# Kernel optimization log

Hardware: AMD Instinct MI355X
Metric: run time of the kernel (lower is better)

## Reference

```python
import jax, jax.numpy as jnp
import numpy as np
from jax import lax

VOCAB, EMB, HID, NCLS, BATCH, SEQ = 32000, 512, 512, 8, 64, 512


def setup_inputs() -> dict:
    key = jax.random.key(0)
    ks = jax.random.split(key, 12)
    s = 0.05
    return {
        "x": jax.random.randint(ks[0], (BATCH, SEQ), 0, VOCAB),
        "emb": jax.random.normal(ks[1], (VOCAB, EMB), jnp.float32) * s,
        "W_ih0": jax.random.normal(ks[2], (HID, EMB), jnp.float32) * s,
        "W_hh0": jax.random.normal(ks[3], (HID, HID), jnp.float32) * s,
        "b_ih0": jax.random.normal(ks[4], (HID,), jnp.float32) * s,
        "b_hh0": jax.random.normal(ks[5], (HID,), jnp.float32) * s,
        "W_ih1": jax.random.normal(ks[6], (HID, HID), jnp.float32) * s,
        "W_hh1": jax.random.normal(ks[7], (HID, HID), jnp.float32) * s,
        "b_ih1": jax.random.normal(ks[8], (HID,), jnp.float32) * s,
        "b_hh1": jax.random.normal(ks[9], (HID,), jnp.float32) * s,
        "fc_W": jax.random.normal(ks[10], (NCLS, HID), jnp.float32) * s,
        "fc_b": jax.random.normal(ks[11], (NCLS,), jnp.float32) * s,
    }


def _rnn_layer(inp, W_ih, W_hh, b_ih, b_hh):
    # inp: [B, S, F]; tanh RNN, batch_first. Precompute input projection once.
    pre = jnp.einsum('bsf,hf->bsh', inp, W_ih) + b_ih + b_hh  # [B,S,H]
    B = inp.shape[0]
    H = W_hh.shape[0]
    h0 = jnp.zeros((B, H), inp.dtype)

    def step(h, p_t):  # p_t: [B,H]
        h = jnp.tanh(p_t + h @ W_hh.T)
        return h, h

    hT, ys = lax.scan(step, h0, pre.transpose(1, 0, 2))  # scan over time
    return ys.transpose(1, 0, 2), hT  # outputs [B,S,H], last hidden [B,H]


def reference(x, emb, W_ih0, W_hh0, b_ih0, b_hh0, W_ih1, W_hh1, b_ih1, b_hh1, fc_W, fc_b):
    xe = emb[x]  # [B,S,E] embedding lookup
    out0, _ = _rnn_layer(xe, W_ih0, W_hh0, b_ih0, b_hh0)
    _, h1 = _rnn_layer(out0, W_ih1, W_hh1, b_ih1, b_hh1)  # hidden[-1]
    return h1 @ fc_W.T + fc_b  # [B, n_class]
```

## Files before the change

kernel.cpp:

```cpp
#include <hip/hip_runtime.h>
#include <stdint.h>


#define BB 64
#define SS 512
#define HH 512

typedef short bf16x8 __attribute__((ext_vector_type(8)));
typedef float f32x4 __attribute__((ext_vector_type(4)));
typedef int i32x4 __attribute__((ext_vector_type(4)));
typedef unsigned int u32;
typedef u32 u32x2 __attribute__((ext_vector_type(2)));

__device__ __forceinline__ unsigned short f2bf(float f) {
  uint32_t u = __builtin_bit_cast(uint32_t, f);
  u += 0x7FFFu + ((u >> 16) & 1u);
  return (unsigned short)(u >> 16);
}
__device__ __forceinline__ float bf2f(unsigned short h) {
  uint32_t u = ((uint32_t)h) << 16;
  return __builtin_bit_cast(float, u);
}
__device__ __forceinline__ int pack2(unsigned short a, unsigned short b) {
  return (int)(unsigned int)a | ((int)(unsigned int)b << 16);
}
__device__ __forceinline__ u32 hipack(u32 a, u32 b) {
  return (a >> 16) | (b & 0xFFFF0000u);
}
__device__ __forceinline__ u32 lopack(u32 a, u32 b) {
  return (a & 0xFFF8u) | ((b & 0xFFF8u) << 16);
}
__device__ __forceinline__ bool tag4(i32x4 v, u32 t) {
  u32 m = (((u32)v[0] ^ t) | ((u32)v[1] ^ t) | ((u32)v[2] ^ t) | ((u32)v[3] ^ t)) & 7u;
  return m == 0u;
}
__device__ __forceinline__ float fast_tanh(float v) {
  float a = __builtin_fabsf(v);
  float e = __expf(-2.0f * a);
  float t = (1.0f - e) / (1.0f + e);
  return __builtin_copysignf(t, v);
}

#define UC_LOAD4(dst, ptr) \
  asm volatile("global_load_dwordx4 %0, %1, off sc0 sc1" : "=v"(dst) : "v"(ptr))
#define UC_LOAD1(dst, ptr) \
  asm volatile("global_load_dword %0, %1, off sc0 sc1" : "=v"(dst) : "v"(ptr))
#define UC_STORE2(ptr, v) \
  asm volatile("global_store_dwordx2 %0, %1, off sc0 sc1" ::"v"(ptr), "v"(v) : "memory")

__global__ __launch_bounds__(512, 2) void k_rnn(
    const int* __restrict__ x, const float* __restrict__ emb,
    const float* __restrict__ Wih0, const float* __restrict__ Whh0,
    const float* __restrict__ bih0, const float* __restrict__ bhh0,
    const float* __restrict__ Wih1, const float* __restrict__ Whh1,
    const float* __restrict__ bih1, const float* __restrict__ bhh1,
    u32* __restrict__ hsl) {
  const int tid = threadIdx.x;
  const int bid = blockIdx.x;
  const int layer = bid >> 5;
  const int lb = bid & 31;
  const int bg = lb >> 3;
  const int c = lb & 7;
  const int wid = tid >> 6;
  const int lane = tid & 63;
  const int kq = wid >> 1;
  const int nh = wid & 1;

  __shared__ __align__(16) unsigned short s_in0[16 * 512];
  __shared__ __align__(16) unsigned short s_Hhi[16 * 512];
  __shared__ __align__(16) unsigned short s_Hlo[16 * 512];
  __shared__ __align__(16) float s_part[4 * 16 * 64];

  const float* Wih = layer ? Wih1 : Wih0;
  const float* Whh = layer ? Whh1 : Whh0;
  const float* bi = layer ? bih1 : bih0;
  const float* bh = layer ? bhh1 : bhh0;

  bf16x8 wih[2][4], whhh[2][4], whhl[2][4];
  {
    const int r16 = lane & 15, kg = lane >> 4;
#pragma unroll
    for (int nt = 0; nt < 2; ++nt) {
#pragma unroll
      for (int kt = 0; kt < 4; ++kt) {
        int row = c * 64 + nh * 32 + nt * 16 + r16;
        int k0 = kq * 128 + kt * 32 + kg * 8;
        const float* p = Wih + row * 512 + k0;
        bf16x8 v;
#pragma unroll
        for (int j = 0; j < 8; ++j) v[j] = (short)f2bf(p[j]);
        wih[nt][kt] = v;
        const float* q = Whh + row * 512 + k0;
        bf16x8 vh, vl;
#pragma unroll
        for (int j = 0; j < 8; ++j) {
          float f = q[j];
          unsigned short h = f2bf(f);
          vh[j] = (short)h;
          vl[j] = (short)f2bf(f - bf2f(h));
        }
        whhh[nt][kt] = vh;
        whhl[nt][kt] = vl;
      }
    }
  }
  float biasv0, biasv1;
  {
    int na = (tid & 31) * 2;
    biasv0 = bi[c * 64 + na] + bh[c * 64 + na];
    biasv1 = bi[c * 64 + na + 1] + bh[c * 64 + na + 1];
  }

  const int r_st = tid >> 5;
  const int ch = tid & 31;

  float4 pf0, pf1, pf2, pf3;
  if (layer == 0) {
    int rid = x[(bg * 16 + r_st) * SS + 0];
    const float4* ep = (const float4*)(emb + (size_t)rid * 512 + ch * 16);
    pf0 = ep[0]; pf1 = ep[1]; pf2 = ep[2]; pf3 = ep[3];
  }

  for (int s = 1; s <= SS; ++s) {
    const u32 exp_h = (u32)((s - 1) & 7);
    const u32* ph = hsl +
        (((size_t)layer * 4 + ((s - 1) & 3)) * 64 + bg * 16 + r_st) * 512 + ch * 16;

    if (layer == 0) {
      i32x4 v0, v1;
      v0[0] = pack2(f2bf(pf0.x), f2bf(pf0.y));
      v0[1] = pack2(f2bf(pf0.z), f2bf(pf0.w));
      v0[2] = pack2(f2bf(pf1.x), f2bf(pf1.y));
      v0[3] = pack2(f2bf(pf1.z), f2bf(pf1.w));
      v1[0] = pack2(f2bf(pf2.x), f2bf(pf2.y));
      v1[1] = pack2(f2bf(pf2.z), f2bf(pf2.w));
      v1[2] = pack2(f2bf(pf3.x), f2bf(pf3.y));
      v1[3] = pack2(f2bf(pf3.z), f2bf(pf3.w));
      *(i32x4*)(s_in0 + r_st * 512 + (((2 * ch) ^ (r_st & 7)) << 3)) = v0;
      *(i32x4*)(s_in0 + r_st * 512 + (((2 * ch + 1) ^ (r_st & 7)) << 3)) = v1;
      if (s < SS) {
        int rid = x[(bg * 16 + r_st) * SS + s];
        const float4* ep = (const float4*)(emb + (size_t)rid * 512 + ch * 16);
        pf0 = ep[0]; pf1 = ep[1]; pf2 = ep[2]; pf3 = ep[3];
      }
    } else {
      i32x4 i0 = {0, 0, 0, 0}, i1 = {0, 0, 0, 0}, i2 = {0, 0, 0, 0}, i3 = {0, 0, 0, 0};
      const u32 exp_i = (u32)(s & 7);
      const u32* pi =
          hsl + (((size_t)(s & 3)) * 64 + bg * 16 + r_st) * 512 + ch * 16;
      while (true) {
        UC_LOAD4(i0, pi);
        UC_LOAD4(i1, pi + 4);
        UC_LOAD4(i2, pi + 8);
        UC_LOAD4(i3, pi + 12);
        asm volatile("s_waitcnt vmcnt(0)"
                     : "+v"(i0), "+v"(i1), "+v"(i2), "+v"(i3)::"memory");
        bool ok = tag4(i0, exp_i) && tag4(i1, exp_i) && tag4(i2, exp_i) &&
                  tag4(i3, exp_i);
        if (__all(ok)) break;
      }
      i32x4 A0 = {(int)hipack(i0[0], i0[1]), (int)hipack(i0[2], i0[3]),
                  (int)hipack(i1[0], i1[1]), (int)hipack(i1[2], i1[3])};
      i32x4 A1 = {(int)hipack(i2[0], i2[1]), (int)hipack(i2[2], i2[3]),
                  (int)hipack(i3[0], i3[1]), (int)hipack(i3[2], i3[3])};
      *(i32x4*)(s_in0 + r_st * 512 + (((2 * ch) ^ (r_st & 7)) << 3)) = A0;
      *(i32x4*)(s_in0 + r_st * 512 + (((2 * ch + 1) ^ (r_st & 7)) << 3)) = A1;
    }
    __syncthreads();

    f32x4 acc0 = {0.f, 0.f, 0.f, 0.f};
    f32x4 acc1 = {0.f, 0.f, 0.f, 0.f};
    {
      const int r16 = lane & 15, kg = lane >> 4;
#pragma unroll
      for (int kt = 0; kt < 4; ++kt) {
        int k8 = kq * 16 + kt * 4 + kg;
        bf16x8 ain = __builtin_bit_cast(
            bf16x8, *(const i32x4*)(s_in0 + r16 * 512 + ((k8 ^ (r16 & 7)) << 3)));
        acc0 = __builtin_amdgcn_mfma_f32_16x16x32_bf16(ain, wih[0][kt], acc0, 0, 0, 0);
        acc1 = __builtin_amdgcn_mfma_f32_16x16x32_bf16(ain, wih[1][kt], acc1, 0, 0, 0);
      }
    }

    if (s > 1) {
      i32x4 h0 = {0, 0, 0, 0}, h1 = {0, 0, 0, 0}, h2 = {0, 0, 0, 0}, h3 = {0, 0, 0, 0};
      if (layer == 0) {
        const bool need_bp = (s > 4) && (tid < 8);
        const u32 exp_bp = (u32)((s - 4) & 7);
        const u32* pbp = hsl + ((size_t)(4 + ((s - 4) & 3)) * 64 + bg * 16) * 512 +
                         (tid < 8 ? tid * 64 : 0);
        while (true) {
          u32 bpw = 0;
          UC_LOAD4(h0, ph);
          UC_LOAD4(h1, ph + 4);
          UC_LOAD4(h2, ph + 8);
          UC_LOAD4(h3, ph + 12);
          UC_LOAD1(bpw, pbp);
          asm volatile("s_waitcnt vmcnt(0)"
                       : "+v"(h0), "+v"(h1), "+v"(h2), "+v"(h3), "+v"(bpw)::"memory");
          bool ok = tag4(h0, exp_h) && tag4(h1, exp_h) && tag4(h2, exp_h) &&
                    tag4(h3, exp_h) && (!need_bp || ((bpw & 7u) == exp_bp));
          if (__all(ok)) break;
        }
      } else {
        while (true) {
          UC_LOAD4(h0, ph);
          UC_LOAD4(h1, ph + 4);
          UC_LOAD4(h2, ph + 8);
          UC_LOAD4(h3, ph + 12);
          asm volatile("s_waitcnt vmcnt(0)"
                       : "+v"(h0), "+v"(h1), "+v"(h2), "+v"(h3)::"memory");
          bool ok = tag4(h0, exp_h) && tag4(h1, exp_h) && tag4(h2, exp_h) &&
                    tag4(h3, exp_h);
          if (__all(ok)) break;
        }
      }
      i32x4 A0 = {(int)hipack(h0[0], h0[1]), (int)hipack(h0[2], h0[3]),
                  (int)hipack(h1[0], h1[1]), (int)hipack(h1[2], h1[3])};
      i32x4 A1 = {(int)hipack(h2[0], h2[1]), (int)hipack(h2[2], h2[3]),
                  (int)hipack(h3[0], h3[1]), (int)hipack(h3[2], h3[3])};
      i32x4 B0 = {(int)lopack(h0[0], h0[1]), (int)lopack(h0[2], h0[3]),
                  (int)lopack(h1[0], h1[1]), (int)lopack(h1[2], h1[3])};
      i32x4 B1v = {(int)lopack(h2[0], h2[1]), (int)lopack(h2[2], h2[3]),
                   (int)lopack(h3[0], h3[1]), (int)lopack(h3[2], h3[3])};
      *(i32x4*)(s_Hhi + r_st * 512 + (((2 * ch) ^ (r_st & 7)) << 3)) = A0;
      *(i32x4*)(s_Hhi + r_st * 512 + (((2 * ch + 1) ^ (r_st & 7)) << 3)) = A1;
      *(i32x4*)(s_Hlo + r_st * 512 + (((2 * ch) ^ (r_st & 7)) << 3)) = B0;
      *(i32x4*)(s_Hlo + r_st * 512 + (((2 * ch + 1) ^ (r_st & 7)) << 3)) = B1v;
    }
    __syncthreads();

    {
      const int r16 = lane & 15, kg = lane >> 4;
      if (s > 1) {
#pragma unroll
        for (int kt = 0; kt < 4; ++kt) {
          int k8 = kq * 16 + kt * 4 + kg;
          bf16x8 ahi = __builtin_bit_cast(
              bf16x8, *(const i32x4*)(s_Hhi + r16 * 512 + ((k8 ^ (r16 & 7)) << 3)));
          bf16x8 alo = __builtin_bit_cast(
              bf16x8, *(const i32x4*)(s_Hlo + r16 * 512 + ((k8 ^ (r16 & 7)) << 3)));
          acc0 = __builtin_amdgcn_mfma_f32_16x16x32_bf16(ahi, whhh[0][kt], acc0, 0, 0, 0);
          acc0 = __builtin_amdgcn_mfma_f32_16x16x32_bf16(ahi, whhl[0][kt], acc0, 0, 0, 0);
          acc0 = __builtin_amdgcn_mfma_f32_16x16x32_bf16(alo, whhh[0][kt], acc0, 0, 0, 0);
          acc1 = __builtin_amdgcn_mfma_f32_16x16x32_bf16(ahi, whhh[1][kt], acc1, 0, 0, 0);
          acc1 = __builtin_amdgcn_mfma_f32_16x16x32_bf16(ahi, whhl[1][kt], acc1, 0, 0, 0);
          acc1 = __builtin_amdgcn_mfma_f32_16x16x32_bf16(alo, whhh[1][kt], acc1, 0, 0, 0);
        }
      }
#pragma unroll
      for (int j = 0; j < 4; ++j) {
        int m = kg * 4 + j;
        int xr = (m >> 2) & 3;
        int n0i = nh * 32 + 0 * 16 + r16;
        int n1i = nh * 32 + 1 * 16 + r16;
        s_part[kq * 1024 + m * 64 + (n0i ^ (xr << 4))] = acc0[j];
        s_part[kq * 1024 + m * 64 + (n1i ^ (xr << 4))] = acc1[j];
      }
    }
    __syncthreads();

    {
      int m = tid >> 5, na = (tid & 31) * 2;
      int xr = (m >> 2) & 3;
      float v0 = biasv0, v1 = biasv1;
#pragma unroll
      for (int q2 = 0; q2 < 4; ++q2) {
        const float2* sp =
            (const float2*)(s_part + q2 * 1024 + m * 64 + (na ^ (xr << 4)));
        float2 t = *sp;
        v0 += t.x;
        v1 += t.y;
      }
      v0 = fast_tanh(v0);
      v1 = fast_tanh(v1);
      unsigned short a0 = f2bf(v0), a1 = f2bf(v1);
      unsigned short b0 = f2bf(v0 - bf2f(a0)), b1 = f2bf(v1 - bf2f(a1));
      u32 tag = (u32)(s & 7);
      u32x2 wv;
      wv[0] = ((u32)a0 << 16) | ((u32)b0 & 0xFFF8u) | tag;
      wv[1] = ((u32)a1 << 16) | ((u32)b1 & 0xFFF8u) | tag;
      u32* dst = hsl + (((size_t)layer * 4 + (s & 3)) * 64 + bg * 16 + m) * 512 +
                 c * 64 + na;
      UC_STORE2(dst, wv);
    }
  }
}

__global__ void k_fc(const u32* __restrict__ h1w, const float* __restrict__ fcW,
                     const float* __restrict__ fcb, float* __restrict__ out) {
  int i = threadIdx.x;
  int b = i >> 3, cc = i & 7;
  float acc = fcb[cc];
  const u32* ph = h1w + b * 512;
  const float* pw = fcW + cc * 512;
  for (int k = 0; k < 512; k += 4) {
    int4 w4 = *(const int4*)(ph + k);
    float4 wv = *(const float4*)(pw + k);
    acc += (bf2f((unsigned short)((u32)w4.x >> 16)) +
            bf2f((unsigned short)((u32)w4.x & 0xFFF8u))) * wv.x;
    acc += (bf2f((unsigned short)((u32)w4.y >> 16)) +
            bf2f((unsigned short)((u32)w4.y & 0xFFF8u))) * wv.y;
    acc += (bf2f((unsigned short)((u32)w4.z >> 16)) +
            bf2f((unsigned short)((u32)w4.z & 0xFFF8u))) * wv.z;
    acc += (bf2f((unsigned short)((u32)w4.w >> 16)) +
            bf2f((unsigned short)((u32)w4.w & 0xFFF8u))) * wv.w;
  }
  out[b * 8 + cc] = acc;
}

extern "C" void kernel_launch(void* const* d_in, const int* in_sizes, int n_in,
                              void* d_out, int out_size, void* d_ws, size_t ws_size,
                              hipStream_t stream) {
  const int* x = (const int*)d_in[0];
  const float* emb = (const float*)d_in[1];
  const float* Wih0 = (const float*)d_in[2];
  const float* Whh0 = (const float*)d_in[3];
  const float* bih0 = (const float*)d_in[4];
  const float* bhh0 = (const float*)d_in[5];
  const float* Wih1 = (const float*)d_in[6];
  const float* Whh1 = (const float*)d_in[7];
  const float* bih1 = (const float*)d_in[8];
  const float* bhh1 = (const float*)d_in[9];
  const float* fcW = (const float*)d_in[10];
  const float* fcb = (const float*)d_in[11];

  u32* hsl = (u32*)d_ws;

  hipMemsetAsync(hsl, 0, (size_t)2 * 4 * 64 * 512 * 4, stream);
  hipLaunchKernelGGL(k_rnn, dim3(64), dim3(512), 0, stream, x, emb, Wih0, Whh0,
                     bih0, bhh0, Wih1, Whh1, bih1, bhh1, hsl);
  hipLaunchKernelGGL(k_fc, dim3(1), dim3(512), 0, stream,
                     hsl + (size_t)4 * 64 * 512, fcW, fcb, (float*)d_out);
}
```

Measured before the change: 2.071 ms.

## Give each wave full K range to drop cross-wave reduction and barrier

Each block now runs 4 waves instead of 8, and each wave owns 16 output columns across the full 512-wide K dimension, holding 16 k-tiles of each weight matrix in registers. This removes the shared-memory partial-sum buffer, one __syncthreads per timestep and the cross-wave reduction. Each wave writes tanh outputs straight to global memory with per-element dword stores. In exchange, per-thread register use triples, each thread loads twice as much h state per step, and each wave runs a longer serial chain of MFMAs, which may lengthen the per-step critical path.

```diff
diff --git a/kernel.cpp b/kernel.cpp
--- a/kernel.cpp
+++ b/kernel.cpp
@@ -10,7 +10,6 @@
 typedef float f32x4 __attribute__((ext_vector_type(4)));
 typedef int i32x4 __attribute__((ext_vector_type(4)));
 typedef unsigned int u32;
-typedef u32 u32x2 __attribute__((ext_vector_type(2)));
 
 __device__ __forceinline__ unsigned short f2bf(float f) {
   uint32_t u = __builtin_bit_cast(uint32_t, f);
@@ -45,10 +44,10 @@
   asm volatile("global_load_dwordx4 %0, %1, off sc0 sc1" : "=v"(dst) : "v"(ptr))
 #define UC_LOAD1(dst, ptr) \
   asm volatile("global_load_dword %0, %1, off sc0 sc1" : "=v"(dst) : "v"(ptr))
-#define UC_STORE2(ptr, v) \
-  asm volatile("global_store_dwordx2 %0, %1, off sc0 sc1" ::"v"(ptr), "v"(v) : "memory")
-
-__global__ __launch_bounds__(512, 2) void k_rnn(
+#define UC_STORE1(ptr, v) \
+  asm volatile("global_store_dword %0, %1, off sc0 sc1" ::"v"(ptr), "v"(v) : "memory")
+
+__global__ __launch_bounds__(256, 1) void k_rnn(
     const int* __restrict__ x, const float* __restrict__ emb,
     const float* __restrict__ Wih0, const float* __restrict__ Whh0,
     const float* __restrict__ bih0, const float* __restrict__ bhh0,
@@ -63,127 +62,138 @@
   const int c = lb & 7;
   const int wid = tid >> 6;
   const int lane = tid & 63;
-  const int kq = wid >> 1;
-  const int nh = wid & 1;
+  const int r16 = lane & 15, kg = lane >> 4;
 
   __shared__ __align__(16) unsigned short s_in0[16 * 512];
   __shared__ __align__(16) unsigned short s_Hhi[16 * 512];
   __shared__ __align__(16) unsigned short s_Hlo[16 * 512];
-  __shared__ __align__(16) float s_part[4 * 16 * 64];
 
   const float* Wih = layer ? Wih1 : Wih0;
   const float* Whh = layer ? Whh1 : Whh0;
   const float* bi = layer ? bih1 : bih0;
   const float* bh = layer ? bhh1 : bhh0;
 
-  bf16x8 wih[2][4], whhh[2][4], whhl[2][4];
+  bf16x8 wih[16], whhh[16], whhl[16];
   {
-    const int r16 = lane & 15, kg = lane >> 4;
-#pragma unroll
-    for (int nt = 0; nt < 2; ++nt) {
-#pragma unroll
-      for (int kt = 0; kt < 4; ++kt) {
-        int row = c * 64 + nh * 32 + nt * 16 + r16;
-        int k0 = kq * 128 + kt * 32 + kg * 8;
-        const float* p = Wih + row * 512 + k0;
-        bf16x8 v;
-#pragma unroll
-        for (int j = 0; j < 8; ++j) v[j] = (short)f2bf(p[j]);
-        wih[nt][kt] = v;
-        const float* q = Whh + row * 512 + k0;
-        bf16x8 vh, vl;
-#pragma unroll
-        for (int j = 0; j < 8; ++j) {
-          float f = q[j];
-          unsigned short h = f2bf(f);
-          vh[j] = (short)h;
-          vl[j] = (short)f2bf(f - bf2f(h));
-        }
-        whhh[nt][kt] = vh;
-        whhl[nt][kt] = vl;
-      }
-    }
-  }
-  float biasv0, biasv1;
+    const int row = c * 64 + wid * 16 + r16;
+#pragma unroll
+    for (int kt = 0; kt < 16; ++kt) {
+      const int k0 = kt * 32 + kg * 8;
+      const float* p = Wih + row * 512 + k0;
+      bf16x8 v;
+#pragma unroll
+      for (int j = 0; j < 8; ++j) v[j] = (short)f2bf(p[j]);
+      wih[kt] = v;
+      const float* q = Whh + row * 512 + k0;
+      bf16x8 vh, vl;
+#pragma unroll
+      for (int j = 0; j < 8; ++j) {
+        float f = q[j];
+        unsigned short h = f2bf(f);
+        vh[j] = (short)h;
+        vl[j] = (short)f2bf(f - bf2f(h));
+      }
+      whhh[kt] = vh;
+      whhl[kt] = vl;
+    }
+  }
+  float bv;
   {
-    int na = (tid & 31) * 2;
-    biasv0 = bi[c * 64 + na] + bh[c * 64 + na];
-    biasv1 = bi[c * 64 + na + 1] + bh[c * 64 + na + 1];
-  }
-
-  const int r_st = tid >> 5;
-  const int ch = tid & 31;
-
-  float4 pf0, pf1, pf2, pf3;
+    const int gcol = c * 64 + wid * 16 + r16;
+    bv = bi[gcol] + bh[gcol];
+  }
+
+  const int r_st = tid >> 4;
+  const int ch = tid & 15;
+
+  float4 pf0, pf1, pf2, pf3, pf4, pf5, pf6, pf7;
   if (layer == 0) {
     int rid = x[(bg * 16 + r_st) * SS + 0];
-    const float4* ep = (const float4*)(emb + (size_t)rid * 512 + ch * 16);
+    const float4* ep = (const float4*)(emb + (size_t)rid * 512 + ch * 32);
     pf0 = ep[0]; pf1 = ep[1]; pf2 = ep[2]; pf3 = ep[3];
+    pf4 = ep[4]; pf5 = ep[5]; pf6 = ep[6]; pf7 = ep[7];
   }
 
   for (int s = 1; s <= SS; ++s) {
     const u32 exp_h = (u32)((s - 1) & 7);
     const u32* ph = hsl +
-        (((size_t)layer * 4 + ((s - 1) & 3)) * 64 + bg * 16 + r_st) * 512 + ch * 16;
+        (((size_t)layer * 4 + ((s - 1) & 3)) * 64 + bg * 16 + r_st) * 512 + ch * 32;
 
     if (layer == 0) {
-      i32x4 v0, v1;
-      v0[0] = pack2(f2bf(pf0.x), f2bf(pf0.y));
-      v0[1] = pack2(f2bf(pf0.z), f2bf(pf0.w));
-      v0[2] = pack2(f2bf(pf1.x), f2bf(pf1.y));
-      v0[3] = pack2(f2bf(pf1.z), f2bf(pf1.w));
-      v1[0] = pack2(f2bf(pf2.x), f2bf(pf2.y));
-      v1[1] = pack2(f2bf(pf2.z), f2bf(pf2.w));
-      v1[2] = pack2(f2bf(pf3.x), f2bf(pf3.y));
-      v1[3] = pack2(f2bf(pf3.z), f2bf(pf3.w));
-      *(i32x4*)(s_in0 + r_st * 512 + (((2 * ch) ^ (r_st & 7)) << 3)) = v0;
-      *(i32x4*)(s_in0 + r_st * 512 + (((2 * ch + 1) ^ (r_st & 7)) << 3)) = v1;
+      i32x4 v0 = {pack2(f2bf(pf0.x), f2bf(pf0.y)), pack2(f2bf(pf0.z), f2bf(pf0.w)),
+                  pack2(f2bf(pf1.x), f2bf(pf1.y)), pack2(f2bf(pf1.z), f2bf(pf1.w))};
+      i32x4 v1 = {pack2(f2bf(pf2.x), f2bf(pf2.y)), pack2(f2bf(pf2.z), f2bf(pf2.w)),
+                  pack2(f2bf(pf3.x), f2bf(pf3.y)), pack2(f2bf(pf3.z), f2bf(pf3.w))};
+      i32x4 v2 = {pack2(f2bf(pf4.x), f2bf(pf4.y)), pack2(f2bf(pf4.z), f2bf(pf4.w)),
+                  pack2(f2bf(pf5.x), f2bf(pf5.y)), pack2(f2bf(pf5.z), f2bf(pf5.w))};
+      i32x4 v3 = {pack2(f2bf(pf6.x), f2bf(pf6.y)), pack2(f2bf(pf6.z), f2bf(pf6.w)),
+                  pack2(f2bf(pf7.x), f2bf(pf7.y)), pack2(f2bf(pf7.z), f2bf(pf7.w))};
+      *(i32x4*)(s_in0 + r_st * 512 + (((ch * 4 + 0) ^ (r_st & 7)) << 3)) = v0;
+      *(i32x4*)(s_in0 + r_st * 512 + (((ch * 4 + 1) ^ (r_st & 7)) << 3)) = v1;
+      *(i32x4*)(s_in0 + r_st * 512 + (((ch * 4 + 2) ^ (r_st & 7)) << 3)) = v2;
+      *(i32x4*)(s_in0 + r_st * 512 + (((ch * 4 + 3) ^ (r_st & 7)) << 3)) = v3;
       if (s < SS) {
         int rid = x[(bg * 16 + r_st) * SS + s];
-        const float4* ep = (const float4*)(emb + (size_t)rid * 512 + ch * 16);
+        const float4* ep = (const float4*)(emb + (size_t)rid * 512 + ch * 32);
         pf0 = ep[0]; pf1 = ep[1]; pf2 = ep[2]; pf3 = ep[3];
+        pf4 = ep[4]; pf5 = ep[5]; pf6 = ep[6]; pf7 = ep[7];
       }
     } else {
       i32x4 i0 = {0, 0, 0, 0}, i1 = {0, 0, 0, 0}, i2 = {0, 0, 0, 0}, i3 = {0, 0, 0, 0};
+      i32x4 i4 = {0, 0, 0, 0}, i5 = {0, 0, 0, 0}, i6 = {0, 0, 0, 0}, i7 = {0, 0, 0, 0};
       const u32 exp_i = (u32)(s & 7);
       const u32* pi =
-          hsl + (((size_t)(s & 3)) * 64 + bg * 16 + r_st) * 512 + ch * 16;
+          hsl + (((size_t)(s & 3)) * 64 + bg * 16 + r_st) * 512 + ch * 32;
       while (true) {
         UC_LOAD4(i0, pi);
         UC_LOAD4(i1, pi + 4);
         UC_LOAD4(i2, pi + 8);
         UC_LOAD4(i3, pi + 12);
+        UC_LOAD4(i4, pi + 16);
+        UC_LOAD4(i5, pi + 20);
+        UC_LOAD4(i6, pi + 24);
+        UC_LOAD4(i7, pi + 28);
         asm volatile("s_waitcnt vmcnt(0)"
-                     : "+v"(i0), "+v"(i1), "+v"(i2), "+v"(i3)::"memory");
+                     : "+v"(i0), "+v"(i1), "+v"(i2), "+v"(i3), "+v"(i4), "+v"(i5),
+                       "+v"(i6), "+v"(i7)::"memory");
         bool ok = tag4(i0, exp_i) && tag4(i1, exp_i) && tag4(i2, exp_i) &&
-                  tag4(i3, exp_i);
+                  tag4(i3, exp_i) && tag4(i4, exp_i) && tag4(i5, exp_i) &&
+                  tag4(i6, exp_i) && tag4(i7, exp_i);
         if (__all(ok)) break;
       }
       i32x4 A0 = {(int)hipack(i0[0], i0[1]), (int)hipack(i0[2], i0[3]),
                   (int)hipack(i1[0], i1[1]), (int)hipack(i1[2], i1[3])};
       i32x4 A1 = {(int)hipack(i2[0], i2[1]), (int)hipack(i2[2], i2[3]),
                   (int)hipack(i3[0], i3[1]), (int)hipack(i3[2], i3[3])};
-      *(i32x4*)(s_in0 + r_st * 512 + (((2 * ch) ^ (r_st & 7)) << 3)) = A0;
-      *(i32x4*)(s_in0 + r_st * 512 + (((2 * ch + 1) ^ (r_st & 7)) << 3)) = A1;
+      i32x4 A2 = {(int)hipack(i4[0], i4[1]), (int)hipack(i4[2], i4[3]),
+                  (int)hipack(i5[0], i5[1]), (int)hipack(i5[2], i5[3])};
+      i32x4 A3 = {(int)hipack(i6[0], i6[1]), (int)hipack(i6[2], i6[3]),
+                  (int)hipack(i7[0], i7[1]), (int)hipack(i7[2], i7[3])};
+      *(i32x4*)(s_in0 + r_st * 512 + (((ch * 4 + 0) ^ (r_st & 7)) << 3)) = A0;
+      *(i32x4*)(s_in0 + r_st * 512 + (((ch * 4 + 1) ^ (r_st & 7)) << 3)) = A1;
+      *(i32x4*)(s_in0 + r_st * 512 + (((ch * 4 + 2) ^ (r_st & 7)) << 3)) = A2;
+      *(i32x4*)(s_in0 + r_st * 512 + (((ch * 4 + 3) ^ (r_st & 7)) << 3)) = A3;
     }
     __syncthreads();
 
     f32x4 acc0 = {0.f, 0.f, 0.f, 0.f};
     f32x4 acc1 = {0.f, 0.f, 0.f, 0.f};
-    {
-      const int r16 = lane & 15, kg = lane >> 4;
-#pragma unroll
-      for (int kt = 0; kt < 4; ++kt) {
-        int k8 = kq * 16 + kt * 4 + kg;
-        bf16x8 ain = __builtin_bit_cast(
-            bf16x8, *(const i32x4*)(s_in0 + r16 * 512 + ((k8 ^ (r16 & 7)) << 3)));
-        acc0 = __builtin_amdgcn_mfma_f32_16x16x32_bf16(ain, wih[0][kt], acc0, 0, 0, 0);
-        acc1 = __builtin_amdgcn_mfma_f32_16x16x32_bf16(ain, wih[1][kt], acc1, 0, 0, 0);
-      }
+    f32x4 acc2 = {0.f, 0.f, 0.f, 0.f};
+    f32x4 acc3 = {0.f, 0.f, 0.f, 0.f};
+#pragma unroll
+    for (int kt = 0; kt < 16; ++kt) {
+      const int k8 = kt * 4 + kg;
+      bf16x8 ain = __builtin_bit_cast(
+          bf16x8, *(const i32x4*)(s_in0 + r16 * 512 + ((k8 ^ (r16 & 7)) << 3)));
+      if ((kt & 3) == 0) acc0 = __builtin_amdgcn_mfma_f32_16x16x32_bf16(ain, wih[kt], acc0, 0, 0, 0);
+      if ((kt & 3) == 1) acc1 = __builtin_amdgcn_mfma_f32_16x16x32_bf16(ain, wih[kt], acc1, 0, 0, 0);
+      if ((kt & 3) == 2) acc2 = __builtin_amdgcn_mfma_f32_16x16x32_bf16(ain, wih[kt], acc2, 0, 0, 0);
+      if ((kt & 3) == 3) acc3 = __builtin_amdgcn_mfma_f32_16x16x32_bf16(ain, wih[kt], acc3, 0, 0, 0);
     }
 
     if (s > 1) {
       i32x4 h0 = {0, 0, 0, 0}, h1 = {0, 0, 0, 0}, h2 = {0, 0, 0, 0}, h3 = {0, 0, 0, 0};
+      i32x4 h4 = {0, 0, 0, 0}, h5 = {0, 0, 0, 0}, h6 = {0, 0, 0, 0}, h7 = {0, 0, 0, 0};
       if (layer == 0) {
         const bool need_bp = (s > 4) && (tid < 8);
         const u32 exp_bp = (u32)((s - 4) & 7);
@@ -195,11 +205,18 @@
           UC_LOAD4(h1, ph + 4);
           UC_LOAD4(h2, ph + 8);
           UC_LOAD4(h3, ph + 12);
+          UC_LOAD4(h4, ph + 16);
+          UC_LOAD4(h5, ph + 20);
+          UC_LOAD4(h6, ph + 24);
+          UC_LOAD4(h7, ph + 28);
           UC_LOAD1(bpw, pbp);
           asm volatile("s_waitcnt vmcnt(0)"
-                       : "+v"(h0), "+v"(h1), "+v"(h2), "+v"(h3), "+v"(bpw)::"memory");
+                       : "+v"(h0), "+v"(h1), "+v"(h2), "+v"(h3), "+v"(h4), "+v"(h5),
+                         "+v"(h6), "+v"(h7), "+v"(bpw)::"memory");
           bool ok = tag4(h0, exp_h) && tag4(h1, exp_h) && tag4(h2, exp_h) &&
-                    tag4(h3, exp_h) && (!need_bp || ((bpw & 7u) == exp_bp));
+                    tag4(h3, exp_h) && tag4(h4, exp_h) && tag4(h5, exp_h) &&
+                    tag4(h6, exp_h) && tag4(h7, exp_h) &&
+                    (!need_bp || ((bpw & 7u) == exp_bp));
           if (__all(ok)) break;
         }
       } else {
@@ -208,10 +225,16 @@
           UC_LOAD4(h1, ph + 4);
           UC_LOAD4(h2, ph + 8);
           UC_LOAD4(h3, ph + 12);
+          UC_LOAD4(h4, ph + 16);
+          UC_LOAD4(h5, ph + 20);
+          UC_LOAD4(h6, ph + 24);
+          UC_LOAD4(h7, ph + 28);
           asm volatile("s_waitcnt vmcnt(0)"
-                       : "+v"(h0), "+v"(h1), "+v"(h2), "+v"(h3)::"memory");
+                       : "+v"(h0), "+v"(h1), "+v"(h2), "+v"(h3), "+v"(h4), "+v"(h5),
+                         "+v"(h6), "+v"(h7)::"memory");
           bool ok = tag4(h0, exp_h) && tag4(h1, exp_h) && tag4(h2, exp_h) &&
-                    tag4(h3, exp_h);
+                    tag4(h3, exp_h) && tag4(h4, exp_h) && tag4(h5, exp_h) &&
+                    tag4(h6, exp_h) && tag4(h7, exp_h);
           if (__all(ok)) break;
         }
       }
@@ -219,70 +242,73 @@
                   (int)hipack(h1[0], h1[1]), (int)hipack(h1[2], h1[3])};
       i32x4 A1 = {(int)hipack(h2[0], h2[1]), (int)hipack(h2[2], h2[3]),
                   (int)hipack(h3[0], h3[1]), (int)hipack(h3[2], h3[3])};
+      i32x4 A2 = {(int)hipack(h4[0], h4[1]), (int)hipack(h4[2], h4[3]),
+                  (int)hipack(h5[0], h5[1]), (int)hipack(h5[2], h5[3])};
+      i32x4 A3 = {(int)hipack(h6[0], h6[1]), (int)hipack(h6[2], h6[3]),
+                  (int)hipack(h7[0], h7[1]), (int)hipack(h7[2], h7[3])};
       i32x4 B0 = {(int)lopack(h0[0], h0[1]), (int)lopack(h0[2], h0[3]),
                   (int)lopack(h1[0], h1[1]), (int)lopack(h1[2], h1[3])};
       i32x4 B1v = {(int)lopack(h2[0], h2[1]), (int)lopack(h2[2], h2[3]),
                    (int)lopack(h3[0], h3[1]), (int)lopack(h3[2], h3[3])};
-      *(i32x4*)(s_Hhi + r_st * 512 + (((2 * ch) ^ (r_st & 7)) << 3)) = A0;
-      *(i32x4*)(s_Hhi + r_st * 512 + (((2 * ch + 1) ^ (r_st & 7)) << 3)) = A1;
-      *(i32x4*)(s_Hlo + r_st * 512 + (((2 * ch) ^ (r_st & 7)) << 3)) = B0;
-      *(i32x4*)(s_Hlo + r_st * 512 + (((2 * ch + 1) ^ (r_st & 7)) << 3)) = B1v;
+      i32x4 B2v = {(int)lopack(h4[0], h4[1]), (int)lopack(h4[2], h4[3]),
+                   (int)lopack(h5[0], h5[1]), (int)lopack(h5[2], h5[3])};
+      i32x4 B3v = {(int)lopack(h6[0], h6[1]), (int)lopack(h6[2], h6[3]),
+                   (int)lopack(h7[0], h7[1]), (int)lopack(h7[2], h7[3])};
+      *(i32x4*)(s_Hhi + r_st * 512 + (((ch * 4 + 0) ^ (r_st & 7)) << 3)) = A0;
+      *(i32x4*)(s_Hhi + r_st * 512 + (((ch * 4 + 1) ^ (r_st & 7)) << 3)) = A1;
+      *(i32x4*)(s_Hhi + r_st * 512 + (((ch * 4 + 2) ^ (r_st & 7)) << 3)) = A2;
+      *(i32x4*)(s_Hhi + r_st * 512 + (((ch * 4 + 3) ^ (r_st & 7)) << 3)) = A3;
+      *(i32x4*)(s_Hlo + r_st * 512 + (((ch * 4 + 0) ^ (r_st & 7)) << 3)) = B0;
+      *(i32x4*)(s_Hlo + r_st * 512 + (((ch * 4 + 1) ^ (r_st & 7)) << 3)) = B1v;
+      *(i32x4*)(s_Hlo + r_st * 512 + (((ch * 4 + 2) ^ (r_st & 7)) << 3)) = B2v;
+      *(i32x4*)(s_Hlo + r_st * 512 + (((ch * 4 + 3) ^ (r_st & 7)) << 3)) = B3v;
     }
     __syncthreads();
 
+    if (s > 1) {
+#pragma unroll
+      for (int kt = 0; kt < 16; ++kt) {
+        const int k8 = kt * 4 + kg;
+        bf16x8 ahi = __builtin_bit_cast(
+            bf16x8, *(const i32x4*)(s_Hhi + r16 * 512 + ((k8 ^ (r16 & 7)) << 3)));
+        bf16x8 alo = __builtin_bit_cast(
+            bf16x8, *(const i32x4*)(s_Hlo + r16 * 512 + ((k8 ^ (r16 & 7)) << 3)));
+        if ((kt & 3) == 0) {
+          acc0 = __builtin_amdgcn_mfma_f32_16x16x32_bf16(ahi, whhh[kt], acc0, 0, 0, 0);
+          acc0 = __builtin_amdgcn_mfma_f32_16x16x32_bf16(ahi, whhl[kt], acc0, 0, 0, 0);
+          acc0 = __builtin_amdgcn_mfma_f32_16x16x32_bf16(alo, whhh[kt], acc0, 0, 0, 0);
+        }
+        if ((kt & 3) == 1) {
+          acc1 = __builtin_amdgcn_mfma_f32_16x16x32_bf16(ahi, whhh[kt], acc1, 0, 0, 0);
+          acc1 = __builtin_amdgcn_mfma_f32_16x16x32_bf16(ahi, whhl[kt], acc1, 0, 0, 0);
+          acc1 = __builtin_amdgcn_mfma_f32_16x16x32_bf16(alo, whhh[kt], acc1, 0, 0, 0);
+        }
+        if ((kt & 3) == 2) {
+          acc2 = __builtin_amdgcn_mfma_f32_16x16x32_bf16(ahi, whhh[kt], acc2, 0, 0, 0);
+          acc2 = __builtin_amdgcn_mfma_f32_16x16x32_bf16(ahi, whhl[kt], acc2, 0, 0, 0);
+          acc2 = __builtin_amdgcn_mfma_f32_16x16x32_bf16(alo, whhh[kt], acc2, 0, 0, 0);
+        }
+        if ((kt & 3) == 3) {
+          acc3 = __builtin_amdgcn_mfma_f32_16x16x32_bf16(ahi, whhh[kt], acc3, 0, 0, 0);
+          acc3 = __builtin_amdgcn_mfma_f32_16x16x32_bf16(ahi, whhl[kt], acc3, 0, 0, 0);
+          acc3 = __builtin_amdgcn_mfma_f32_16x16x32_bf16(alo, whhh[kt], acc3, 0, 0, 0);
+        }
+      }
+    }
+
     {
-      const int r16 = lane & 15, kg = lane >> 4;
-      if (s > 1) {
-#pragma unroll
-        for (int kt = 0; kt < 4; ++kt) {
-          int k8 = kq * 16 + kt * 4 + kg;
-          bf16x8 ahi = __builtin_bit_cast(
-              bf16x8, *(const i32x4*)(s_Hhi + r16 * 512 + ((k8 ^ (r16 & 7)) << 3)));
-          bf16x8 alo = __builtin_bit_cast(
-              bf16x8, *(const i32x4*)(s_Hlo + r16 * 512 + ((k8 ^ (r16 & 7)) << 3)));
-          acc0 = __builtin_amdgcn_mfma_f32_16x16x32_bf16(ahi, whhh[0][kt], acc0, 0, 0, 0);
-          acc0 = __builtin_amdgcn_mfma_f32_16x16x32_bf16(ahi, whhl[0][kt], acc0, 0, 0, 0);
-          acc0 = __builtin_amdgcn_mfma_f32_16x16x32_bf16(alo, whhh[0][kt], acc0, 0, 0, 0);
-          acc1 = __builtin_amdgcn_mfma_f32_16x16x32_bf16(ahi, whhh[1][kt], acc1, 0, 0, 0);
-          acc1 = __builtin_amdgcn_mfma_f32_16x16x32_bf16(ahi, whhl[1][kt], acc1, 0, 0, 0);
-          acc1 = __builtin_amdgcn_mfma_f32_16x16x32_bf16(alo, whhh[1][kt], acc1, 0, 0, 0);
-        }
-      }
+      f32x4 fa = acc0 + acc1 + acc2 + acc3;
+      const u32 tag = (u32)(s & 7);
+      u32* dst = hsl + (((size_t)layer * 4 + (s & 3)) * 64 + bg * 16 + kg * 4) * 512 +
+                 c * 64 + wid * 16 + r16;
 #pragma unroll
       for (int j = 0; j < 4; ++j) {
-        int m = kg * 4 + j;
-        int xr = (m >> 2) & 3;
-        int n0i = nh * 32 + 0 * 16 + r16;
-        int n1i = nh * 32 + 1 * 16 + r16;
-        s_part[kq * 1024 + m * 64 + (n0i ^ (xr << 4))] = acc0[j];
-        s_part[kq * 1024 + m * 64 + (n1i ^ (xr << 4))] = acc1[j];
-      }
-    }
-    __syncthreads();
-
-    {
-      int m = tid >> 5, na = (tid & 31) * 2;
-      int xr = (m >> 2) & 3;
-      float v0 = biasv0, v1 = biasv1;
-#pragma unroll
-      for (int q2 = 0; q2 < 4; ++q2) {
-        const float2* sp =
-            (const float2*)(s_part + q2 * 1024 + m * 64 + (na ^ (xr << 4)));
-        float2 t = *sp;
-        v0 += t.x;
-        v1 += t.y;
-      }
-      v0 = fast_tanh(v0);
-      v1 = fast_tanh(v1);
-      unsigned short a0 = f2bf(v0), a1 = f2bf(v1);
-      unsigned short b0 = f2bf(v0 - bf2f(a0)), b1 = f2bf(v1 - bf2f(a1));
-      u32 tag = (u32)(s & 7);
-      u32x2 wv;
-      wv[0] = ((u32)a0 << 16) | ((u32)b0 & 0xFFF8u) | tag;
-      wv[1] = ((u32)a1 << 16) | ((u32)b1 & 0xFFF8u) | tag;
-      u32* dst = hsl + (((size_t)layer * 4 + (s & 3)) * 64 + bg * 16 + m) * 512 +
-                 c * 64 + na;
-      UC_STORE2(dst, wv);
+        float t = fast_tanh(fa[j] + bv);
+        unsigned short a = f2bf(t);
+        unsigned short b = f2bf(t - bf2f(a));
+        u32 wv = ((u32)a << 16) | ((u32)b & 0xFFF8u) | tag;
+        UC_STORE1(dst + j * 512, wv);
+      }
     }
   }
 }
@@ -328,7 +354,7 @@
   u32* hsl = (u32*)d_ws;
 
   hipMemsetAsync(hsl, 0, (size_t)2 * 4 * 64 * 512 * 4, stream);
-  hipLaunchKernelGGL(k_rnn, dim3(64), dim3(512), 0, stream, x, emb, Wih0, Whh0,
+  hipLaunchKernelGGL(k_rnn, dim3(64), dim3(256), 0, stream, x, emb, Wih0, Whh0,
                      bih0, bhh0, Wih1, Whh1, bih1, bhh1, hsl);
   hipLaunchKernelGGL(k_fc, dim3(1), dim3(512), 0, stream,
                      hsl + (size_t)4 * 64 * 512, fcW, fcb, (float*)d_out);
```

New measurement: 2.798 ms. 35.1% more time.

## Use LDS-only barriers, split MFMA accumulators, and defer embedding prefetch

Applied to the files above, without the earlier changes.

Three of the per-step __syncthreads calls become an LDS-only wait plus s_barrier, so the barriers no longer wait on outstanding global loads. This lets the embedding prefetch, now issued after the input-projection MFMAs, stay in flight across the barriers. The recurrent MFMAs accumulate into six independent accumulators instead of two serial chains, which shortens dependency latency; the partial sums are added at the end. The risk is different floating-point summation order and more register pressure, though the launch bounds of 512 threads and 2 blocks already constrain registers.

```diff
diff --git a/kernel.cpp b/kernel.cpp
--- a/kernel.cpp
+++ b/kernel.cpp
@@ -40,6 +40,12 @@
   float t = (1.0f - e) / (1.0f + e);
   return __builtin_copysignf(t, v);
 }
+
+#define BAR_LDS()                                            \
+  do {                                                       \
+    asm volatile("s_waitcnt lgkmcnt(0)" ::: "memory");       \
+    __builtin_amdgcn_s_barrier();                            \
+  } while (0)
 
 #define UC_LOAD4(dst, ptr) \
   asm volatile("global_load_dwordx4 %0, %1, off sc0 sc1" : "=v"(dst) : "v"(ptr))
@@ -65,6 +71,7 @@
   const int lane = tid & 63;
   const int kq = wid >> 1;
   const int nh = wid & 1;
+  const int r16 = lane & 15, kg = lane >> 4;
 
   __shared__ __align__(16) unsigned short s_in0[16 * 512];
   __shared__ __align__(16) unsigned short s_Hhi[16 * 512];
@@ -78,7 +85,6 @@
 
   bf16x8 wih[2][4], whhh[2][4], whhl[2][4];
   {
-    const int r16 = lane & 15, kg = lane >> 4;
 #pragma unroll
     for (int nt = 0; nt < 2; ++nt) {
 #pragma unroll
@@ -125,6 +131,9 @@
     const u32 exp_h = (u32)((s - 1) & 7);
     const u32* ph = hsl +
         (((size_t)layer * 4 + ((s - 1) & 3)) * 64 + bg * 16 + r_st) * 512 + ch * 16;
+
+    int nrid = 0;
+    if (layer == 0 && s < SS) nrid = x[(bg * 16 + r_st) * SS + s];
 
     if (layer == 0) {
       i32x4 v0, v1;
@@ -138,11 +147,6 @@
       v1[3] = pack2(f2bf(pf3.z), f2bf(pf3.w));
       *(i32x4*)(s_in0 + r_st * 512 + (((2 * ch) ^ (r_st & 7)) << 3)) = v0;
       *(i32x4*)(s_in0 + r_st * 512 + (((2 * ch + 1) ^ (r_st & 7)) << 3)) = v1;
-      if (s < SS) {
-        int rid = x[(bg * 16 + r_st) * SS + s];
-        const float4* ep = (const float4*)(emb + (size_t)rid * 512 + ch * 16);
-        pf0 = ep[0]; pf1 = ep[1]; pf2 = ep[2]; pf3 = ep[3];
-      }
     } else {
       i32x4 i0 = {0, 0, 0, 0}, i1 = {0, 0, 0, 0}, i2 = {0, 0, 0, 0}, i3 = {0, 0, 0, 0};
       const u32 exp_i = (u32)(s & 7);
@@ -166,22 +170,28 @@
       *(i32x4*)(s_in0 + r_st * 512 + (((2 * ch) ^ (r_st & 7)) << 3)) = A0;
       *(i32x4*)(s_in0 + r_st * 512 + (((2 * ch + 1) ^ (r_st & 7)) << 3)) = A1;
     }
-    __syncthreads();
-
-    f32x4 acc0 = {0.f, 0.f, 0.f, 0.f};
-    f32x4 acc1 = {0.f, 0.f, 0.f, 0.f};
-    {
-      const int r16 = lane & 15, kg = lane >> 4;
-#pragma unroll
-      for (int kt = 0; kt < 4; ++kt) {
-        int k8 = kq * 16 + kt * 4 + kg;
-        bf16x8 ain = __builtin_bit_cast(
-            bf16x8, *(const i32x4*)(s_in0 + r16 * 512 + ((k8 ^ (r16 & 7)) << 3)));
-        acc0 = __builtin_amdgcn_mfma_f32_16x16x32_bf16(ain, wih[0][kt], acc0, 0, 0, 0);
-        acc1 = __builtin_amdgcn_mfma_f32_16x16x32_bf16(ain, wih[1][kt], acc1, 0, 0, 0);
-      }
-    }
-
+    BAR_LDS();
+
+    f32x4 a0i = {0.f, 0.f, 0.f, 0.f};
+    f32x4 a1i = {0.f, 0.f, 0.f, 0.f};
+#pragma unroll
+    for (int kt = 0; kt < 4; ++kt) {
+      int k8 = kq * 16 + kt * 4 + kg;
+      bf16x8 ain = __builtin_bit_cast(
+          bf16x8, *(const i32x4*)(s_in0 + r16 * 512 + ((k8 ^ (r16 & 7)) << 3)));
+      a0i = __builtin_amdgcn_mfma_f32_16x16x32_bf16(ain, wih[0][kt], a0i, 0, 0, 0);
+      a1i = __builtin_amdgcn_mfma_f32_16x16x32_bf16(ain, wih[1][kt], a1i, 0, 0, 0);
+    }
+
+    if (layer == 0 && s < SS) {
+      const float4* ep = (const float4*)(emb + (size_t)nrid * 512 + ch * 16);
+      pf0 = ep[0]; pf1 = ep[1]; pf2 = ep[2]; pf3 = ep[3];
+    }
+
+    f32x4 a0hh = {0.f, 0.f, 0.f, 0.f}, a0hl = {0.f, 0.f, 0.f, 0.f},
+          a0lh = {0.f, 0.f, 0.f, 0.f};
+    f32x4 a1hh = {0.f, 0.f, 0.f, 0.f}, a1hl = {0.f, 0.f, 0.f, 0.f},
+          a1lh = {0.f, 0.f, 0.f, 0.f};
     if (s > 1) {
       i32x4 h0 = {0, 0, 0, 0}, h1 = {0, 0, 0, 0}, h2 = {0, 0, 0, 0}, h3 = {0, 0, 0, 0};
       if (layer == 0) {
@@ -228,26 +238,28 @@
       *(i32x4*)(s_Hlo + r_st * 512 + (((2 * ch) ^ (r_st & 7)) << 3)) = B0;
       *(i32x4*)(s_Hlo + r_st * 512 + (((2 * ch + 1) ^ (r_st & 7)) << 3)) = B1v;
     }
-    __syncthreads();
+    BAR_LDS();
+
+    if (s > 1) {
+#pragma unroll
+      for (int kt = 0; kt < 4; ++kt) {
+        int k8 = kq * 16 + kt * 4 + kg;
+        bf16x8 ahi = __builtin_bit_cast(
+            bf16x8, *(const i32x4*)(s_Hhi + r16 * 512 + ((k8 ^ (r16 & 7)) << 3)));
+        bf16x8 alo = __builtin_bit_cast(
+            bf16x8, *(const i32x4*)(s_Hlo + r16 * 512 + ((k8 ^ (r16 & 7)) << 3)));
+        a0hh = __builtin_amdgcn_mfma_f32_16x16x32_bf16(ahi, whhh[0][kt], a0hh, 0, 0, 0);
+        a0hl = __builtin_amdgcn_mfma_f32_16x16x32_bf16(ahi, whhl[0][kt], a0hl, 0, 0, 0);
+        a0lh = __builtin_amdgcn_mfma_f32_16x16x32_bf16(alo, whhh[0][kt], a0lh, 0, 0, 0);
+        a1hh = __builtin_amdgcn_mfma_f32_16x16x32_bf16(ahi, whhh[1][kt], a1hh, 0, 0, 0);
+        a1hl = __builtin_amdgcn_mfma_f32_16x16x32_bf16(ahi, whhl[1][kt], a1hl, 0, 0, 0);
+        a1lh = __builtin_amdgcn_mfma_f32_16x16x32_bf16(alo, whhh[1][kt], a1lh, 0, 0, 0);
+      }
+    }
 
     {
-      const int r16 = lane & 15, kg = lane >> 4;
-      if (s > 1) {
-#pragma unroll
-        for (int kt = 0; kt < 4; ++kt) {
-          int k8 = kq * 16 + kt * 4 + kg;
-          bf16x8 ahi = __builtin_bit_cast(
-              bf16x8, *(const i32x4*)(s_Hhi + r16 * 512 + ((k8 ^ (r16 & 7)) << 3)));
-          bf16x8 alo = __builtin_bit_cast(
-              bf16x8, *(const i32x4*)(s_Hlo + r16 * 512 + ((k8 ^ (r16 & 7)) << 3)));
-          acc0 = __builtin_amdgcn_mfma_f32_16x16x32_bf16(ahi, whhh[0][kt], acc0, 0, 0, 0);
-          acc0 = __builtin_amdgcn_mfma_f32_16x16x32_bf16(ahi, whhl[0][kt], acc0, 0, 0, 0);
-          acc0 = __builtin_amdgcn_mfma_f32_16x16x32_bf16(alo, whhh[0][kt], acc0, 0, 0, 0);
-          acc1 = __builtin_amdgcn_mfma_f32_16x16x32_bf16(ahi, whhh[1][kt], acc1, 0, 0, 0);
-          acc1 = __builtin_amdgcn_mfma_f32_16x16x32_bf16(ahi, whhl[1][kt], acc1, 0, 0, 0);
-          acc1 = __builtin_amdgcn_mfma_f32_16x16x32_bf16(alo, whhh[1][kt], acc1, 0, 0, 0);
-        }
-      }
+      f32x4 acc0 = (a0i + a0hh) + (a0hl + a0lh);
+      f32x4 acc1 = (a1i + a1hh) + (a1hl + a1lh);
 #pragma unroll
       for (int j = 0; j < 4; ++j) {
         int m = kg * 4 + j;
@@ -258,7 +270,7 @@
         s_part[kq * 1024 + m * 64 + (n1i ^ (xr << 4))] = acc1[j];
       }
     }
-    __syncthreads();
+    BAR_LDS();
 
     {
       int m = tid >> 5, na = (tid & 31) * 2;
```

New measurement: 2.085 ms. Within noise of the previous version (+0.6%).
